# Kernel optimization log

Measured on AMD Instinct MI355X. Metric: run time of the kernel, lower is better.

## Reference

```python
import jax, jax.numpy as jnp
import numpy as np

D_MODEL = 2048
N_HEADS = 16
HEAD_DIM = D_MODEL // N_HEADS  # 128
MAX_POS = 2048


def _precompute_cos_sin(max_pos, head_dim):
    inv_freq = 1.0 / (10000.0 ** (jnp.arange(0, head_dim, 2, dtype=jnp.float32) / head_dim))
    t = jnp.arange(max_pos, dtype=jnp.float32)
    freqs = jnp.outer(t, inv_freq)          # [max_pos, head_dim//2]
    emb = jnp.concatenate([freqs, freqs], axis=-1)  # [max_pos, head_dim]
    return jnp.cos(emb), jnp.sin(emb)


def _rotate_half(x):
    x1, x2 = x[..., : x.shape[-1] // 2], x[..., x.shape[-1] // 2 :]
    return jnp.concatenate([-x2, x1], axis=-1)


def setup_inputs() -> dict:
    key = jax.random.key(0)
    kx, kq, kk, kv, ko = jax.random.split(key, 5)
    B, S = 2, 2048
    x = jax.random.normal(kx, (B, S, D_MODEL), dtype=jnp.float32)
    scale = 1.0 / np.sqrt(D_MODEL)
    # torch Linear weights are [out_features, in_features]
    Wq = jax.random.normal(kq, (D_MODEL, D_MODEL), dtype=jnp.float32) * scale
    Wk = jax.random.normal(kk, (D_MODEL, D_MODEL), dtype=jnp.float32) * scale
    Wv = jax.random.normal(kv, (D_MODEL, D_MODEL), dtype=jnp.float32) * scale
    Wo = jax.random.normal(ko, (D_MODEL, D_MODEL), dtype=jnp.float32) * scale
    cos, sin = _precompute_cos_sin(MAX_POS, HEAD_DIM)
    # causal mask: True where attention is disallowed (masked_fill semantics)
    mask = jnp.triu(jnp.ones((S, S), dtype=bool), k=1)
    mask = jnp.broadcast_to(mask[None], (B, S, S))
    return {"x": x, "Wq": Wq, "Wk": Wk, "Wv": Wv, "Wo": Wo,
            "cos": cos, "sin": sin, "mask": mask}


def reference(x, Wq, Wk, Wv, Wo, cos, sin, mask):
    B, S, _ = x.shape
    H, Dh = N_HEADS, HEAD_DIM
    scaling = Dh ** -0.5

    def split_heads(y):  # [B,S,D] -> [B,H,S,Dh]
        return y.reshape(B, S, H, Dh).transpose(0, 2, 1, 3)

    q = split_heads(x @ Wq.T)
    k = split_heads(x @ Wk.T)
    v = split_heads(x @ Wv.T)

    c = cos[:S][None, None]  # [1,1,S,Dh]
    s = sin[:S][None, None]
    q = q * c + _rotate_half(q) * s
    k = k * c + _rotate_half(k) * s

    scores = jnp.einsum("bhqd,bhkd->bhqk", q, k) * scaling
    scores = jnp.where(mask[:, None], -jnp.inf, scores)
    attn = jax.nn.softmax(scores, axis=-1)
    out = jnp.einsum("bhqk,bhkd->bhqd", attn, v)  # [B,H,S,Dh]
    out = out.transpose(0, 2, 1, 3).reshape(B, S, H * Dh)
    return out @ Wo.T
```

## Files before the change

### kernel.cpp

```cpp
#include <hip/hip_runtime.h>

typedef float f32x4 __attribute__((ext_vector_type(4)));
typedef short s16x8 __attribute__((ext_vector_type(8)));
typedef unsigned short u16;
typedef u16 u16x4 __attribute__((ext_vector_type(4)));

#define SEQ 2048
#define BATCH 2
#define NH 16
#define DH 128
#define DM 2048
#define MROWS (BATCH * SEQ)

__device__ constexpr float SCALE2 = 0.12751879523531f;

__device__ __forceinline__ u16 f2bf(float f) {
  unsigned u = __float_as_uint(f);
  u += 0x7fffu + ((u >> 16) & 1u);
  return (u16)(u >> 16);
}
__device__ __forceinline__ float bf2f(u16 b) {
  return __uint_as_float(((unsigned)b) << 16);
}

__device__ __forceinline__ void gld_lds16(const void* g, void* l) {
  __builtin_amdgcn_global_load_lds(
      (const __attribute__((address_space(1))) unsigned int*)g,
      (__attribute__((address_space(3))) unsigned int*)l, 16, 0, 0);
}

__global__ __launch_bounds__(256) void cast_all(const float* __restrict__ x,
                                                const float* __restrict__ Wq,
                                                const float* __restrict__ Wk,
                                                const float* __restrict__ Wv,
                                                const float* __restrict__ Wo,
                                                u16* __restrict__ xb,
                                                u16* __restrict__ Wqkvb,
                                                u16* __restrict__ Wob) {
  long i = (long)blockIdx.x * 256 + threadIdx.x;
  const float* src;
  u16* dst;
  long off;
  if (i < 2097152)      { src = x;  dst = xb;              off = i; }
  else if (i < 3145728) { src = Wq; dst = Wqkvb;           off = i - 2097152; }
  else if (i < 4194304) { src = Wk; dst = Wqkvb + 4194304; off = i - 3145728; }
  else if (i < 5242880) { src = Wv; dst = Wqkvb + 8388608; off = i - 4194304; }
  else                  { src = Wo; dst = Wob;             off = i - 5242880; }
  float4 v = ((const float4*)src)[off];
  u16x4 o;
  o[0] = f2bf(v.x); o[1] = f2bf(v.y); o[2] = f2bf(v.z); o[3] = f2bf(v.w);
  ((u16x4*)dst)[off] = o;
}


template <bool F32OUT>
__global__ __launch_bounds__(256) void gemm_bt(const u16* __restrict__ A,
                                               const u16* __restrict__ B,
                                               void* __restrict__ Cv,
                                               int M, int N, int K) {
  __shared__ u16 As[128 * 32];
  __shared__ u16 Bs[128 * 32];
  const int tid = threadIdx.x;
  const int wave = tid >> 6;
  const int lane = tid & 63;
  const int r = lane & 15, g = lane >> 4;

  const int mtiles = M >> 7;
  const int nwg = mtiles * (N >> 7);
  const int cpx = nwg >> 3;
  const int bid = blockIdx.x;
  const int swz = (bid & 7) * cpx + (bid >> 3);
  const int m0 = (swz % mtiles) * 128;
  const int n0 = (swz / mtiles) * 128;

  const int wm = (wave >> 1) * 64;
  const int wn = (wave & 1) * 64;

  f32x4 acc[4][4] = {};

  const int row0 = tid >> 2;
  const int col0 = (tid & 3) * 8;
  const u16* ga0 = A + (long)(m0 + row0) * K + col0;
  const u16* ga1 = A + (long)(m0 + 64 + row0) * K + col0;
  const u16* gb0 = B + (long)(n0 + row0) * K + col0;
  const u16* gb1 = B + (long)(n0 + 64 + row0) * K + col0;

  u16* lA0 = &As[wave * 512];
  u16* lA1 = &As[2048 + wave * 512];
  u16* lB0 = &Bs[wave * 512];
  u16* lB1 = &Bs[2048 + wave * 512];

  for (int k0 = 0; k0 < K; k0 += 32) {
    gld_lds16(ga0 + k0, lA0);
    gld_lds16(ga1 + k0, lA1);
    gld_lds16(gb0 + k0, lB0);
    gld_lds16(gb1 + k0, lB1);
    __syncthreads();
    s16x8 af[4], bfr[4];
#pragma unroll
    for (int i = 0; i < 4; i++) {
      af[i]  = *(const s16x8*)&As[(wm + i * 16 + r) * 32 + g * 8];
      bfr[i] = *(const s16x8*)&Bs[(wn + i * 16 + r) * 32 + g * 8];
    }
#pragma unroll
    for (int i = 0; i < 4; i++)
#pragma unroll
      for (int j = 0; j < 4; j++)
        acc[i][j] = __builtin_amdgcn_mfma_f32_16x16x32_bf16(af[i], bfr[j], acc[i][j], 0, 0, 0);
    __syncthreads();
  }

  float* Cf = (float*)Cv;
  u16* Cb = (u16*)Cv;
#pragma unroll
  for (int i = 0; i < 4; i++)
#pragma unroll
    for (int j = 0; j < 4; j++) {
      const int row = m0 + wm + i * 16 + g * 4;
      const int col = n0 + wn + j * 16 + r;
#pragma unroll
      for (int q = 0; q < 4; q++) {
        float v = acc[i][j][q];
        if (F32OUT) Cf[(long)(row + q) * N + col] = v;
        else        Cb[(long)(row + q) * N + col] = f2bf(v);
      }
    }
}

__global__ __launch_bounds__(256) void gemm_qkv(const u16* __restrict__ A,
                                                const u16* __restrict__ B,
                                                u16* __restrict__ Qo,
                                                u16* __restrict__ Ko,
                                                u16* __restrict__ Vo) {
  __shared__ u16 As[128 * 32];
  __shared__ u16 Bs[128 * 32];
  const int tid = threadIdx.x;
  const int wave = tid >> 6;
  const int lane = tid & 63;
  const int r = lane & 15, g = lane >> 4;

  const int bid = blockIdx.x;
  const int swz = (bid & 7) * 192 + (bid >> 3);
  const int m0 = (swz & 31) * 128;
  const int n0 = (swz >> 5) * 128;

  const int wm = (wave >> 1) * 64;
  const int wn = (wave & 1) * 64;

  f32x4 acc[4][4] = {};

  const int row0 = tid >> 2;
  const int col0 = (tid & 3) * 8;
  const u16* ga0 = A + (long)(m0 + row0) * 2048 + col0;
  const u16* ga1 = A + (long)(m0 + 64 + row0) * 2048 + col0;
  const u16* gb0 = B + (long)(n0 + row0) * 2048 + col0;
  const u16* gb1 = B + (long)(n0 + 64 + row0) * 2048 + col0;

  u16* lA0 = &As[wave * 512];
  u16* lA1 = &As[2048 + wave * 512];
  u16* lB0 = &Bs[wave * 512];
  u16* lB1 = &Bs[2048 + wave * 512];

  for (int k0 = 0; k0 < 2048; k0 += 32) {
    gld_lds16(ga0 + k0, lA0);
    gld_lds16(ga1 + k0, lA1);
    gld_lds16(gb0 + k0, lB0);
    gld_lds16(gb1 + k0, lB1);
    __syncthreads();
    s16x8 af[4], bfr[4];
#pragma unroll
    for (int i = 0; i < 4; i++) {
      af[i]  = *(const s16x8*)&As[(wm + i * 16 + r) * 32 + g * 8];
      bfr[i] = *(const s16x8*)&Bs[(wn + i * 16 + r) * 32 + g * 8];
    }
#pragma unroll
    for (int i = 0; i < 4; i++)
#pragma unroll
      for (int j = 0; j < 4; j++)
        acc[i][j] = __builtin_amdgcn_mfma_f32_16x16x32_bf16(af[i], bfr[j], acc[i][j], 0, 0, 0);
    __syncthreads();
  }

  u16* Cb = (n0 < 2048) ? Qo : (n0 < 4096 ? Ko : Vo);
  const int nc0 = n0 & 2047;
#pragma unroll
  for (int i = 0; i < 4; i++)
#pragma unroll
    for (int j = 0; j < 4; j++) {
      const int row = m0 + wm + i * 16 + g * 4;
      const int col = nc0 + wn + j * 16 + r;
#pragma unroll
      for (int q = 0; q < 4; q++)
        Cb[(long)(row + q) * 2048 + col] = f2bf(acc[i][j][q]);
    }
}

__global__ __launch_bounds__(256) void rope_kernel(u16* __restrict__ Q, u16* __restrict__ K,
                                                   const float* __restrict__ cosT,
                                                   const float* __restrict__ sinT) {
  int idx = blockIdx.x * 256 + threadIdx.x;
  int d = idx & 63;
  int h = (idx >> 6) & 15;
  int s = (idx >> 10) & 2047;
  int b = idx >> 21;
  float c = cosT[s * DH + d];
  float sn = sinT[s * DH + d];
  long base = ((long)(b * SEQ + s)) * DM + h * DH + d;
  float q1 = bf2f(Q[base]), q2 = bf2f(Q[base + 64]);
  Q[base]      = f2bf(q1 * c - q2 * sn);
  Q[base + 64] = f2bf(q2 * c + q1 * sn);
  float k1 = bf2f(K[base]), k2 = bf2f(K[base + 64]);
  K[base]      = f2bf(k1 * c - k2 * sn);
  K[base + 64] = f2bf(k2 * c + k1 * sn);
}

__global__ __launch_bounds__(256) void transpose_v(const u16* __restrict__ Vlin,
                                                   u16* __restrict__ Vt) {
  __shared__ u16 tile[64][129];
  int t = threadIdx.x;
  int st = blockIdx.x & 31;
  int h = (blockIdx.x >> 5) & 15;
  int b = blockIdx.x >> 9;
  int s0 = st * 64;
  const u16* src = Vlin + ((long)(b * SEQ + s0)) * DM + h * DH;
#pragma unroll
  for (int rr = 0; rr < 4; rr++) {
    int row = rr * 16 + (t >> 4);
    int col = (t & 15) * 8;
    s16x8 v = *(const s16x8*)&src[(long)row * DM + col];
#pragma unroll
    for (int j = 0; j < 8; j++) tile[row][col + j] = (u16)v[j];
  }
  __syncthreads();
  u16* dst = Vt + ((long)(b * NH + h)) * DH * SEQ + s0;
#pragma unroll
  for (int rr = 0; rr < 4; rr++) {
    int d = rr * 32 + (t >> 3);
    int sc = (t & 7) * 8;
    s16x8 o;
#pragma unroll
    for (int j = 0; j < 8; j++) o[j] = (short)tile[sc + j][d];
    *(s16x8*)&dst[(long)d * SEQ + sc] = o;
  }
}


__device__ __forceinline__ void softmax_swapped(
    f32x4 (&s)[4], float& mi, float& li,
    u16 (&pl)[16][64], float (&als)[16],
    int qbase, int k0, int r, int g) {
  const int q = qbase + r;
  const bool edge = (k0 + 63) > qbase;
  float v[16];
#pragma unroll
  for (int kk = 0; kk < 4; kk++)
#pragma unroll
    for (int i = 0; i < 4; i++) {
      float x = s[kk][i] * SCALE2;
      if (edge && (k0 + kk * 16 + g * 4 + i > q)) x = -1e30f;
      v[kk * 4 + i] = x;
    }
  float t8[8], t4[4];
#pragma unroll
  for (int j = 0; j < 8; j++) t8[j] = fmaxf(v[2 * j], v[2 * j + 1]);
#pragma unroll
  for (int j = 0; j < 4; j++) t4[j] = fmaxf(t8[2 * j], t8[2 * j + 1]);
  float mx = fmaxf(fmaxf(t4[0], t4[1]), fmaxf(t4[2], t4[3]));
  mx = fmaxf(mx, __shfl_xor(mx, 16, 64));
  mx = fmaxf(mx, __shfl_xor(mx, 32, 64));
  const float mnew = fmaxf(mi, mx);
  const float a = exp2f(mi - mnew);
  float p[16];
#pragma unroll
  for (int j = 0; j < 16; j++) p[j] = exp2f(v[j] - mnew);
  float s8[8], s4[4];
#pragma unroll
  for (int j = 0; j < 8; j++) s8[j] = p[2 * j] + p[2 * j + 1];
#pragma unroll
  for (int j = 0; j < 4; j++) s4[j] = s8[2 * j] + s8[2 * j + 1];
  float ps = (s4[0] + s4[1]) + (s4[2] + s4[3]);
  ps += __shfl_xor(ps, 16, 64);
  ps += __shfl_xor(ps, 32, 64);
  li = li * a + ps;
  mi = mnew;
  const int sw = (r & 7) << 3;
#pragma unroll
  for (int kk = 0; kk < 4; kk++) {
    u16x4 w;
#pragma unroll
    for (int i = 0; i < 4; i++) w[i] = f2bf(p[kk * 4 + i]);
    *(u16x4*)&pl[r][(kk * 16 + g * 4) ^ sw] = w;
  }
  als[r] = a;
}

__global__ __launch_bounds__(512, 4) void attn_kernel(const u16* __restrict__ Q,
                                                      const u16* __restrict__ K,
                                                      const u16* __restrict__ Vt,
                                                      u16* __restrict__ O) {
  __shared__ u16 Klds[64 * 128];
  __shared__ u16 Vlds[128 * 64];
  __shared__ u16 Plds[8][16][64];
  __shared__ float Alds[8][16];

  const int tid = threadIdx.x, wave = tid >> 6, lane = tid & 63;
  const int r = lane & 15, g = lane >> 4;
  const int bh = blockIdx.x & 31;
  const int j = blockIdx.x >> 5;
  const int h = bh & 15, b = bh >> 4;
  const bool isB = wave >= 4;
  const int w4 = wave & 3;
  const int strip = isB ? (31 - j) : j;
  const int q0 = strip * 64 + w4 * 16;
  const int nt = 32 - j;
  const int lastA = j;

  const u16* Qbh = Q + (long)b * SEQ * DM + h * DH;
  const u16* Kbh = K + (long)b * SEQ * DM + h * DH;
  const u16* Vbh = Vt + ((long)(b * NH + h)) * DH * SEQ;

  s16x8 qf[4];
#pragma unroll
  for (int jj = 0; jj < 4; jj++)
    qf[jj] = *(const s16x8*)&Qbh[(long)(q0 + r) * DM + jj * 32 + g * 8];

  f32x4 oacc[8] = {};
  float mi = -1e30f, li = 0.f;

  for (int kt = 0; kt < nt; ++kt) {
    const int k0 = kt * 64;
    __syncthreads();
#pragma unroll
    for (int c = 0; c < 2; ++c) {
      const int s = c * 512 + tid;
      const int krow = s >> 4;
      const int kch = (s & 15) ^ (krow & 7);
      gld_lds16(Kbh + (long)(k0 + krow) * DM + kch * 8,
                &Klds[(c * 512 + wave * 64) * 8]);
      const int vrow = s >> 3;
      const int vch = (s & 7) ^ (vrow & 7);
      gld_lds16(Vbh + (long)vrow * SEQ + k0 + vch * 8,
                &Vlds[(c * 512 + wave * 64) * 8]);
    }
    __syncthreads();

    const bool active = isB || (kt <= lastA);
    if (active) {
      f32x4 sacc[4] = {};
#pragma unroll
      for (int kk = 0; kk < 4; kk++) {
#pragma unroll
        for (int jj = 0; jj < 4; jj++) {
          s16x8 kf = *(const s16x8*)&Klds[(kk * 16 + r) * 128 +
                                          (((jj * 4 + g) ^ (r & 7)) * 8)];
          sacc[kk] = __builtin_amdgcn_mfma_f32_16x16x32_bf16(kf, qf[jj], sacc[kk], 0, 0, 0);
        }
      }
      softmax_swapped(sacc, mi, li, Plds[wave], Alds[wave], q0, k0, r, g);

      f32x4 av = *(const f32x4*)&Alds[wave][g * 4];
#pragma unroll
      for (int f = 0; f < 8; f++)
#pragma unroll
        for (int i = 0; i < 4; i++) oacc[f][i] *= av[i];

      const int sw = (r & 7) << 3;
#pragma unroll
      for (int kc = 0; kc < 2; kc++) {
        s16x8 pf = *(const s16x8*)&Plds[wave][r][(kc * 32 + g * 8) ^ sw];
#pragma unroll
        for (int f = 0; f < 8; f++) {
          s16x8 vf = *(const s16x8*)&Vlds[(f * 16 + r) * 64 +
                                          (((kc * 4 + g) ^ (r & 7)) * 8)];
          oacc[f] = __builtin_amdgcn_mfma_f32_16x16x32_bf16(pf, vf, oacc[f], 0, 0, 0);
        }
      }
    }
  }

  Alds[wave][r] = 1.f / li;
  f32x4 iv = *(const f32x4*)&Alds[wave][g * 4];
  u16* Obh = O + (long)b * SEQ * DM + h * DH;
#pragma unroll
  for (int f = 0; f < 8; f++)
#pragma unroll
    for (int i = 0; i < 4; i++)
      Obh[(long)(q0 + g * 4 + i) * DM + f * 16 + r] = f2bf(oacc[f][i] * iv[i]);
}

extern "C" void kernel_launch(void* const* d_in, const int* in_sizes, int n_in,
                              void* d_out, int out_size, void* d_ws, size_t ws_size,
                              hipStream_t stream) {
  const float* x    = (const float*)d_in[0];
  const float* Wq   = (const float*)d_in[1];
  const float* Wk   = (const float*)d_in[2];
  const float* Wv   = (const float*)d_in[3];
  const float* Wo   = (const float*)d_in[4];
  const float* cosT = (const float*)d_in[5];
  const float* sinT = (const float*)d_in[6];

  if (ws_size < (size_t)134217728) return;

  char* ws = (char*)d_ws;
  u16* xb    = (u16*)(ws);
  u16* Wqkvb = (u16*)(ws + 16777216);
  u16* Wob   = (u16*)(ws + 41943040);
  u16* Qlin  = (u16*)(ws + 50331648);
  u16* Klin  = (u16*)(ws + 67108864);
  u16* Vlin  = (u16*)(ws + 83886080);
  u16* Vt    = (u16*)(ws + 100663296);
  u16* Olin  = (u16*)(ws + 117440512);

  cast_all<<<24576, 256, 0, stream>>>(x, Wq, Wk, Wv, Wo, xb, Wqkvb, Wob);

  gemm_qkv<<<1536, 256, 0, stream>>>(xb, Wqkvb, Qlin, Klin, Vlin);

  rope_kernel<<<16384, 256, 0, stream>>>(Qlin, Klin, cosT, sinT);
  transpose_v<<<1024, 256, 0, stream>>>(Vlin, Vt);
  attn_kernel<<<512, 512, 0, stream>>>(Qlin, Klin, Vt, Olin);

  gemm_bt<true><<<512, 256, 0, stream>>>(Olin, Wob, d_out, MROWS, DM, DM);
}
```

Baseline: 295.3 us.

## Rewrite QKV GEMM as 256x256 double-buffered 8-wave pipelined kernel

Replaces the 128x128 single-buffered QKV projection GEMM with a 256x256 tile, 512-thread kernel. It uses double-buffered LDS with K-tiles of 64, XOR-swizzled LDS layout to avoid bank conflicts, and four interleaved compute phases that each prefetch the next tile's quarter while MFMAs run, with setprio around the MFMA bursts. This aims to hide global load latency and raise reuse per LDS byte. In exchange it uses 128KB of LDS and many accumulator registers, so occupancy is low, and the tuned waitcnt/barrier choreography is fragile.

```diff
diff --git a/kernel.cpp b/kernel.cpp
--- a/kernel.cpp
+++ b/kernel.cpp
@@ -52,7 +52,6 @@
   ((u16x4*)dst)[off] = o;
 }
 
-
 template <bool F32OUT>
 __global__ __launch_bounds__(256) void gemm_bt(const u16* __restrict__ A,
                                                const u16* __restrict__ B,
@@ -127,72 +126,101 @@
     }
 }
 
-__global__ __launch_bounds__(256) void gemm_qkv(const u16* __restrict__ A,
-                                                const u16* __restrict__ B,
-                                                u16* __restrict__ Qo,
-                                                u16* __restrict__ Ko,
-                                                u16* __restrict__ Vo) {
-  __shared__ u16 As[128 * 32];
-  __shared__ u16 Bs[128 * 32];
-  const int tid = threadIdx.x;
-  const int wave = tid >> 6;
-  const int lane = tid & 63;
+__global__ __launch_bounds__(512, 2) void gemm_qkv8(const u16* __restrict__ A,
+                                                    const u16* __restrict__ B,
+                                                    u16* __restrict__ Qo,
+                                                    u16* __restrict__ Ko,
+                                                    u16* __restrict__ Vo) {
+  __shared__ u16 Alds[2][256 * 64];
+  __shared__ u16 Blds[2][256 * 64];
+  const int tid = threadIdx.x, wave = tid >> 6, lane = tid & 63;
   const int r = lane & 15, g = lane >> 4;
-
+  const int wm = wave >> 2, wn = wave & 3;
   const int bid = blockIdx.x;
-  const int swz = (bid & 7) * 192 + (bid >> 3);
-  const int m0 = (swz & 31) * 128;
-  const int n0 = (swz >> 5) * 128;
-
-  const int wm = (wave >> 1) * 64;
-  const int wn = (wave & 1) * 64;
-
-  f32x4 acc[4][4] = {};
-
-  const int row0 = tid >> 2;
-  const int col0 = (tid & 3) * 8;
-  const u16* ga0 = A + (long)(m0 + row0) * 2048 + col0;
-  const u16* ga1 = A + (long)(m0 + 64 + row0) * 2048 + col0;
-  const u16* gb0 = B + (long)(n0 + row0) * 2048 + col0;
-  const u16* gb1 = B + (long)(n0 + 64 + row0) * 2048 + col0;
-
-  u16* lA0 = &As[wave * 512];
-  u16* lA1 = &As[2048 + wave * 512];
-  u16* lB0 = &Bs[wave * 512];
-  u16* lB1 = &Bs[2048 + wave * 512];
-
-  for (int k0 = 0; k0 < 2048; k0 += 32) {
-    gld_lds16(ga0 + k0, lA0);
-    gld_lds16(ga1 + k0, lA1);
-    gld_lds16(gb0 + k0, lB0);
-    gld_lds16(gb1 + k0, lB1);
-    __syncthreads();
-    s16x8 af[4], bfr[4];
-#pragma unroll
-    for (int i = 0; i < 4; i++) {
-      af[i]  = *(const s16x8*)&As[(wm + i * 16 + r) * 32 + g * 8];
-      bfr[i] = *(const s16x8*)&Bs[(wn + i * 16 + r) * 32 + g * 8];
-    }
-#pragma unroll
-    for (int i = 0; i < 4; i++)
-#pragma unroll
-      for (int j = 0; j < 4; j++)
-        acc[i][j] = __builtin_amdgcn_mfma_f32_16x16x32_bf16(af[i], bfr[j], acc[i][j], 0, 0, 0);
-    __syncthreads();
-  }
+  const int swz = (bid & 7) * 48 + (bid >> 3);
+  const int m0 = (swz & 15) * 256;
+  const int n0 = (swz >> 4) * 256;
+
+  const int lrow = lane >> 3;
+  const int csrc = (lane & 7) ^ lrow;
+
+  f32x4 acc[8][4] = {};
+
+#define STAGE_A(TA, MH, BUF) do {                                             \
+  _Pragma("unroll") for (int i_ = 0; i_ < 2; ++i_) {                          \
+    const int band_ = i_ * 128 + (MH) * 64 + wave * 8;                        \
+    gld_lds16(A + (long)(m0 + band_ + lrow) * 2048 + (TA) * 64 + csrc * 8,    \
+              &Alds[BUF][band_ * 64]);                                        \
+  } } while (0)
+#define STAGE_B(TA, NH, BUF) do {                                             \
+  _Pragma("unroll") for (int i_ = 0; i_ < 2; ++i_) {                          \
+    const int rb_ = (2 * i_ + (wave >> 2)) * 64 + (NH) * 32 + (wave & 3) * 8; \
+    gld_lds16(B + (long)(n0 + rb_ + lrow) * 2048 + (TA) * 64 + csrc * 8,      \
+              &Blds[BUF][rb_ * 64]);                                          \
+  } } while (0)
+
+  STAGE_A(0, 0, 0); STAGE_B(0, 0, 0); STAGE_A(0, 1, 0); STAGE_B(0, 1, 0);
+  STAGE_A(1, 0, 1); STAGE_B(1, 0, 1);
+  asm volatile("s_waitcnt vmcnt(4)" ::: "memory");
+  __builtin_amdgcn_s_barrier();
+
+#define PHASE(MH, NH, ...) do {                                               \
+  const u16* Ab_ = Alds[bt]; const u16* Bb_ = Blds[bt];                       \
+  s16x8 a_[4][2], b_[2][2];                                                   \
+  _Pragma("unroll") for (int mf = 0; mf < 4; ++mf)                            \
+    _Pragma("unroll") for (int kk = 0; kk < 2; ++kk) {                        \
+      const int arow = wm * 128 + (MH) * 64 + mf * 16 + r;                    \
+      a_[mf][kk] = *(const s16x8*)&Ab_[arow * 64 +                            \
+                                       (((kk * 4 + g) ^ (arow & 7)) * 8)];    \
+    }                                                                         \
+  _Pragma("unroll") for (int nf = 0; nf < 2; ++nf)                            \
+    _Pragma("unroll") for (int kk = 0; kk < 2; ++kk) {                        \
+      const int brow = wn * 64 + (NH) * 32 + nf * 16 + r;                     \
+      b_[nf][kk] = *(const s16x8*)&Bb_[brow * 64 +                            \
+                                       (((kk * 4 + g) ^ (brow & 7)) * 8)];    \
+    }                                                                         \
+  __VA_ARGS__;                                                                \
+  __builtin_amdgcn_s_barrier();                                               \
+  asm volatile("s_waitcnt lgkmcnt(0)" ::: "memory");                          \
+  __builtin_amdgcn_sched_barrier(0);                                          \
+  __builtin_amdgcn_s_setprio(1);                                              \
+  _Pragma("unroll") for (int mf = 0; mf < 4; ++mf)                            \
+    _Pragma("unroll") for (int nf = 0; nf < 2; ++nf)                          \
+      _Pragma("unroll") for (int kk = 0; kk < 2; ++kk)                        \
+        acc[(MH) * 4 + mf][(NH) * 2 + nf] =                                   \
+            __builtin_amdgcn_mfma_f32_16x16x32_bf16(                          \
+                a_[mf][kk], b_[nf][kk],                                       \
+                acc[(MH) * 4 + mf][(NH) * 2 + nf], 0, 0, 0);                  \
+  __builtin_amdgcn_s_setprio(0);                                              \
+} while (0)
+
+  for (int t = 0; t < 32; ++t) {
+    const int bt = t & 1, bn = bt ^ 1;
+    PHASE(0, 0, if (t < 31) STAGE_A(t + 1, 1, bn));
+    __builtin_amdgcn_s_barrier();
+    PHASE(0, 1, if (t < 31) STAGE_B(t + 1, 1, bn));
+    __builtin_amdgcn_s_barrier();
+    PHASE(1, 0, if (t < 30) STAGE_A(t + 2, 0, bt));
+    __builtin_amdgcn_s_barrier();
+    PHASE(1, 1, if (t < 30) STAGE_B(t + 2, 0, bt));
+    if (t < 30)       asm volatile("s_waitcnt vmcnt(4)" ::: "memory");
+    else if (t == 30) asm volatile("s_waitcnt vmcnt(0)" ::: "memory");
+    __builtin_amdgcn_s_barrier();
+  }
+#undef PHASE
+#undef STAGE_A
+#undef STAGE_B
 
   u16* Cb = (n0 < 2048) ? Qo : (n0 < 4096 ? Ko : Vo);
   const int nc0 = n0 & 2047;
 #pragma unroll
-  for (int i = 0; i < 4; i++)
-#pragma unroll
-    for (int j = 0; j < 4; j++) {
-      const int row = m0 + wm + i * 16 + g * 4;
-      const int col = nc0 + wn + j * 16 + r;
-#pragma unroll
-      for (int q = 0; q < 4; q++)
-        Cb[(long)(row + q) * 2048 + col] = f2bf(acc[i][j][q]);
-    }
+  for (int mi = 0; mi < 8; ++mi)
+#pragma unroll
+    for (int ni = 0; ni < 4; ++ni)
+#pragma unroll
+      for (int q = 0; q < 4; ++q)
+        Cb[(long)(m0 + wm * 128 + mi * 16 + g * 4 + q) * 2048 +
+           nc0 + wn * 64 + ni * 16 + r] = f2bf(acc[mi][ni][q]);
 }
 
 __global__ __launch_bounds__(256) void rope_kernel(u16* __restrict__ Q, u16* __restrict__ K,
@@ -413,7 +441,7 @@
 
   cast_all<<<24576, 256, 0, stream>>>(x, Wq, Wk, Wv, Wo, xb, Wqkvb, Wob);
 
-  gemm_qkv<<<1536, 256, 0, stream>>>(xb, Wqkvb, Qlin, Klin, Vlin);
+  gemm_qkv8<<<384, 512, 0, stream>>>(xb, Wqkvb, Qlin, Klin, Vlin);
 
   rope_kernel<<<16384, 256, 0, stream>>>(Qlin, Klin, cosT, sinT);
   transpose_v<<<1024, 256, 0, stream>>>(Vlin, Vt);
```

Result: slower. 337.4 us (+14.3%).
